# Kernel optimization log

Measured on AMD Instinct MI355X. Metric: run time of the kernel, lower is better.

## Reference

```python
import jax, jax.numpy as jnp
import numpy as np

EMB, HEADS, T_BLK = 1024, 16, 2048
B, T = 2, 2048
HD = EMB // HEADS


def setup_inputs() -> dict:
    key = jax.random.key(0)
    ks = jax.random.split(key, 9)
    s = 1.0 / np.sqrt(EMB)
    return {
        "x": jax.random.normal(ks[0], (B, T, EMB), jnp.float32),
        "Wq": jax.random.normal(ks[1], (EMB, EMB), jnp.float32) * s,
        "bq": jax.random.normal(ks[2], (EMB,), jnp.float32) * s,
        "Wk": jax.random.normal(ks[3], (EMB, EMB), jnp.float32) * s,
        "bk": jax.random.normal(ks[4], (EMB,), jnp.float32) * s,
        "Wv": jax.random.normal(ks[5], (EMB, EMB), jnp.float32) * s,
        "bv": jax.random.normal(ks[6], (EMB,), jnp.float32) * s,
        "Wo": jax.random.normal(ks[7], (EMB, EMB), jnp.float32) * s,
        "bo": jax.random.normal(ks[8], (EMB,), jnp.float32) * s,
    }


def reference(x, Wq, bq, Wk, bk, Wv, bv, Wo, bo):
    # eval mode: dropout is identity
    Bn, Tn, C = x.shape
    def proj(W, b):
        y = x @ W.T + b                      # [B,T,C]
        return y.reshape(Bn, Tn, HEADS, HD).transpose(0, 2, 1, 3)  # [B,H,T,hd]
    q, k, v = proj(Wq, bq), proj(Wk, bk), proj(Wv, bv)
    scores = jnp.einsum('bhqd,bhkd->bhqk', q, k) * (HD ** -0.5)  # [B,H,T,T]
    causal = jnp.tril(jnp.ones((Tn, Tn), dtype=bool))
    scores = jnp.where(causal, scores, -jnp.inf)
    w = jax.nn.softmax(scores, axis=-1)
    out = jnp.einsum('bhqk,bhkd->bhqd', w, v)                    # [B,H,T,hd]
    out = out.transpose(0, 2, 1, 3).reshape(Bn, Tn, C)
    return out @ Wo.T + bo
```

## Files before the change

kernel.cpp:

```cpp
#include <hip/hip_runtime.h>
#include <stdint.h>

#define EMB   1024
#define HEADS 16
#define HD    64
#define BB    2
#define TT    2048
#define MTOT  (BB*TT)
#define LDA   72

#define ELX (4194304u)
#define ELW (1048576u)

#define CSCALE (0.125f * 1.44269504088896f)

typedef __attribute__((ext_vector_type(8))) short short8;
typedef __attribute__((ext_vector_type(4))) float f32x4;
typedef __attribute__((ext_vector_type(4))) unsigned short us4;

__device__ __forceinline__ float bf2f(ushort u) {
  union { uint32_t u; float f; } x; x.u = ((uint32_t)u) << 16; return x.f;
}
__device__ __forceinline__ ushort f2bf(float f) {
  union { float f; uint32_t u; } x; x.f = f;
  uint32_t u = x.u;
  u += 0x7fffu + ((u >> 16) & 1u);
  return (ushort)(u >> 16);
}
__device__ __forceinline__ ushort f2bf_trunc(float f) {
  union { float f; uint32_t u; } x; x.f = f;
  return (ushort)(x.u >> 16);
}
__device__ __forceinline__ uint32_t pack2(uint32_t lo, uint32_t hi) {
  return (lo >> 16) | (hi & 0xFFFF0000u);
}
__device__ __forceinline__ short8 pack8(f32x4 a, f32x4 b) {
  union { f32x4 v; uint32_t u[4]; } A, B;
  A.v = a; B.v = b;
  union { uint32_t d[4]; short8 s; } R;
  R.d[0] = pack2(A.u[0], A.u[1]);
  R.d[1] = pack2(A.u[2], A.u[3]);
  R.d[2] = pack2(B.u[0], B.u[1]);
  R.d[3] = pack2(B.u[2], B.u[3]);
  return R.s;
}

__device__ __forceinline__ short8 cvt8_rne(const float* f) {
  f32x4 a = *(const f32x4*)f;
  f32x4 b = *(const f32x4*)(f + 4);
  short8 r;
  r[0] = (short)f2bf(a[0]); r[1] = (short)f2bf(a[1]);
  r[2] = (short)f2bf(a[2]); r[3] = (short)f2bf(a[3]);
  r[4] = (short)f2bf(b[0]); r[5] = (short)f2bf(b[1]);
  r[6] = (short)f2bf(b[2]); r[7] = (short)f2bf(b[3]);
  return r;
}

__global__ void detect_dtype(const uint32_t* __restrict__ x, int* __restrict__ flag) {
  if (threadIdx.x == 0) {
    int cnt = 0;
    for (int i = 0; i < 256; ++i) {
      uint32_t lo = x[i] & 0xFFFFu;
      uint32_t e = (lo >> 7) & 0xFFu;
      if (e >= 0x70u && e <= 0x8Fu) ++cnt;
    }
    *flag = (cnt > 128) ? 1 : 0;
  }
}

__global__ __launch_bounds__(256) void convert3(const void* __restrict__ w0,
                                                const void* __restrict__ w1,
                                                const void* __restrict__ w2,
                                                ushort* __restrict__ dst,
                                                const int* __restrict__ flag) {
  const size_t i = ((size_t)blockIdx.x * 256 + threadIdx.x) * 8;
  const int wi = (int)(i >> 20);
  const size_t off = i & (ELW - 1);
  const void* src = (wi == 0) ? w0 : (wi == 1) ? w1 : w2;
  if (*flag) *(short8*)(dst + i) = *(const short8*)((const ushort*)src + off);
  else       *(short8*)(dst + i) = cvt8_rne((const float*)src + off);
}

template<bool BF> struct PF {
  short8 b0, b1;
  f32x4 f0, f1, f2, f3;
  __device__ __forceinline__ void load(const void* base, size_t i0, size_t i1) {
    if constexpr (BF) {
      b0 = *(const short8*)((const ushort*)base + i0);
      b1 = *(const short8*)((const ushort*)base + i1);
    } else {
      const float* p0 = (const float*)base + i0;
      const float* p1 = (const float*)base + i1;
      f0 = *(const f32x4*)p0; f1 = *(const f32x4*)(p0 + 4);
      f2 = *(const f32x4*)p1; f3 = *(const f32x4*)(p1 + 4);
    }
  }
  __device__ __forceinline__ void store(ushort* l0, ushort* l1) {
    if constexpr (BF) { *(short8*)l0 = b0; *(short8*)l1 = b1; }
    else { *(short8*)l0 = pack8(f0, f1); *(short8*)l1 = pack8(f2, f3); }
  }
};

template<bool ABF, bool WBF>
__device__ __forceinline__ void gemm_pipe128(const void* __restrict__ Ap,
                                             const void* __restrict__ Bp,
                                             int m0, int n0,
                                             ushort* As, ushort* Ws,
                                             f32x4 acc[4][4]) {
  const int tid  = threadIdx.x;
  const int w    = tid >> 6;
  const int lane = tid & 63;
  const int quad = lane >> 4;
  const int l16  = lane & 15;
  const int wrow = w >> 1, wcol = w & 1;
  const int srow = tid >> 2;
  const int scol = (tid & 3) * 8;

  const size_t a0 = (size_t)(m0 + srow) * EMB + scol;
  const size_t a1 = (size_t)(m0 + srow + 64) * EMB + scol;
  const size_t b0 = (size_t)(n0 + srow) * EMB + scol;
  const size_t b1 = (size_t)(n0 + srow + 64) * EMB + scol;

  PF<ABF> pa; PF<WBF> pb;
  pa.load(Ap, a0, a1);
  pb.load(Bp, b0, b1);

  for (int k0 = 0; k0 < EMB; k0 += 32) {
    __syncthreads();
    pa.store(&As[srow * 32 + scol], &As[(srow + 64) * 32 + scol]);
    pb.store(&Ws[srow * 32 + scol], &Ws[(srow + 64) * 32 + scol]);
    if (k0 + 32 < EMB) {
      pa.load(Ap, a0 + k0 + 32, a1 + k0 + 32);
      pb.load(Bp, b0 + k0 + 32, b1 + k0 + 32);
    }
    __syncthreads();

    short8 af[4], bfr[4];
#pragma unroll
    for (int i = 0; i < 4; ++i)
      af[i]  = *(const short8*)&As[(wrow * 64 + i * 16 + l16) * 32 + quad * 8];
#pragma unroll
    for (int i = 0; i < 4; ++i)
      bfr[i] = *(const short8*)&Ws[(wcol * 64 + i * 16 + l16) * 32 + quad * 8];
#pragma unroll
    for (int mi = 0; mi < 4; ++mi)
#pragma unroll
      for (int ni = 0; ni < 4; ++ni)
        acc[mi][ni] = __builtin_amdgcn_mfma_f32_16x16x32_bf16(af[mi], bfr[ni], acc[mi][ni], 0, 0, 0);
  }
}

__device__ __forceinline__ void qkv_epilogue(f32x4 acc[4][4], int mt, int n0, int mat,
                                             const void* bias, int isbf,
                                             ushort* qo, ushort* ko, ushort* vo) {
  const int tid  = threadIdx.x;
  const int w    = tid >> 6;
  const int lane = tid & 63;
  const int quad = lane >> 4;
  const int l16  = lane & 15;
  const int wrow = w >> 1, wcol = w & 1;
  ushort* dst = (mat == 0) ? qo : ko;
  const float sc = (mat == 0) ? CSCALE : 1.0f;

#pragma unroll
  for (int ni = 0; ni < 4; ++ni) {
    const int n = n0 + wcol * 64 + ni * 16 + l16;
    const float bv_ = isbf ? bf2f(((const ushort*)bias)[n]) : ((const float*)bias)[n];
    const int hh = n >> 6, d = n & 63;
#pragma unroll
    for (int mi = 0; mi < 4; ++mi) {
      const int mbase = mt * 128 + wrow * 64 + mi * 16 + quad * 4;
      const int b = mbase >> 11, t = mbase & (TT - 1);
      if (mat == 2) {
        us4 pk;
#pragma unroll
        for (int r = 0; r < 4; ++r) pk[r] = f2bf(acc[mi][ni][r] + bv_);
        *(us4*)&vo[((size_t)((b * HEADS + hh) * HD + d)) * TT + t] = pk;
      } else {
#pragma unroll
        for (int r = 0; r < 4; ++r)
          dst[((size_t)((b * HEADS + hh) * TT + t + r)) * HD + d] = f2bf((acc[mi][ni][r] + bv_) * sc);
      }
    }
  }
}

__global__ __launch_bounds__(256) void qkv_pipe(const void* __restrict__ x,
                                                const ushort* __restrict__ w3,
                                                const void* __restrict__ bq,
                                                const void* __restrict__ bk,
                                                const void* __restrict__ bv,
                                                ushort* __restrict__ qo,
                                                ushort* __restrict__ ko,
                                                ushort* __restrict__ vo,
                                                const int* __restrict__ flag) {
  __shared__ __align__(16) ushort As[128 * 32];
  __shared__ __align__(16) ushort Ws[128 * 32];
  const int nt = blockIdx.x % 24;
  const int mt = blockIdx.x / 24;
  const int mat = nt >> 3;
  const int n0  = (nt & 7) * 128;
  const ushort* W  = w3 + (size_t)mat * ELW;
  const void* bias = (mat == 0) ? bq : (mat == 1) ? bk : bv;

  f32x4 acc[4][4];
#pragma unroll
  for (int i = 0; i < 4; ++i)
#pragma unroll
    for (int j = 0; j < 4; ++j) acc[i][j] = (f32x4){0.f, 0.f, 0.f, 0.f};

  const int isbf = *flag;
  if (isbf) gemm_pipe128<true,  true>(x, W, mt * 128, n0, As, Ws, acc);
  else      gemm_pipe128<false, true>(x, W, mt * 128, n0, As, Ws, acc);
  qkv_epilogue(acc, mt, n0, mat, bias, isbf, qo, ko, vo);
}

__global__ __launch_bounds__(256) void attn3(const ushort* __restrict__ qw,
                                             const ushort* __restrict__ kw,
                                             const ushort* __restrict__ vtw,
                                             ushort* __restrict__ out) {
  __shared__ __align__(16) ushort Ks[64 * LDA];
  __shared__ __align__(16) ushort Vts[64 * LDA];
  __shared__ __align__(16) ushort Ps[4][16 * LDA];

  const int bid = blockIdx.x;
  const int j  = bid >> 8;
  const int r8 = bid & 255;
  const int qh = r8 & 31;
  const int bh = j * 8 + (r8 >> 5);
  int qt;
  if      (j == 0) qt = qh;
  else if (j == 1) qt = 31 - qh;
  else if (j == 2) qt = (qh + 16) & 31;
  else             qt = 31 - ((qh + 16) & 31);
  const int h = bh & (HEADS - 1);
  const int b = bh >> 4;

  const int tid  = threadIdx.x;
  const int w    = tid >> 6;
  const int lane = tid & 63;
  const int quad = lane >> 4;
  const int l16  = lane & 15;

  const size_t hoff = ((size_t)(b * HEADS + h)) * TT * HD;
  const ushort* Qg = qw + hoff;
  const ushort* Kg = kw + hoff;
  const ushort* Vg = vtw + hoff;
  const int q0 = qt * 64;

  short8 qf[2];
  {
    const ushort* qrow = Qg + (size_t)(q0 + w * 16 + l16) * HD;
    qf[0] = *(const short8*)(qrow + quad * 8);
    qf[1] = *(const short8*)(qrow + 32 + quad * 8);
  }

  const int row = tid >> 2;
  const int c0  = (tid & 3) * 16;
  const ushort* Kbase = Kg + (size_t)row * HD + c0;
  const ushort* Vbase = Vg + (size_t)row * TT + c0;

  short8 pk0 = *(const short8*)(Kbase);
  short8 pk1 = *(const short8*)(Kbase + 8);
  short8 pv0 = *(const short8*)(Vbase);
  short8 pv1 = *(const short8*)(Vbase + 8);

  float ls[4] = {0.f, 0.f, 0.f, 0.f};
  f32x4 O[4];
#pragma unroll
  for (int ni = 0; ni < 4; ++ni) O[ni] = (f32x4){0.f, 0.f, 0.f, 0.f};

  for (int kt = 0; kt <= qt; ++kt) {
    const int k0 = kt * 64;
    __syncthreads();
    *(short8*)&Ks[row * LDA + c0]      = pk0;
    *(short8*)&Ks[row * LDA + c0 + 8]  = pk1;
    *(short8*)&Vts[row * LDA + c0]     = pv0;
    *(short8*)&Vts[row * LDA + c0 + 8] = pv1;
    if (kt < qt) {
      const size_t ko_ = (size_t)(k0 + 64) * HD;
      pk0 = *(const short8*)(Kbase + ko_);
      pk1 = *(const short8*)(Kbase + ko_ + 8);
      pv0 = *(const short8*)(Vbase + k0 + 64);
      pv1 = *(const short8*)(Vbase + k0 + 64 + 8);
    }
    __syncthreads();

    f32x4 s[4];
#pragma unroll
    for (int ni = 0; ni < 4; ++ni) s[ni] = (f32x4){0.f, 0.f, 0.f, 0.f};
#pragma unroll
    for (int ks = 0; ks < 2; ++ks) {
#pragma unroll
      for (int ni = 0; ni < 4; ++ni) {
        short8 kb = *(const short8*)&Ks[(ni * 16 + l16) * LDA + ks * 32 + quad * 8];
        s[ni] = __builtin_amdgcn_mfma_f32_16x16x32_bf16(qf[ks], kb, s[ni], 0, 0, 0);
      }
    }

    if (kt == qt) {
#pragma unroll
      for (int ni = 0; ni < 4; ++ni) {
        const int kk = k0 + ni * 16 + l16;
#pragma unroll
        for (int r = 0; r < 4; ++r) {
          const int qq = q0 + w * 16 + quad * 4 + r;
          if (kk > qq) s[ni][r] = -__builtin_inff();
        }
      }
    }

#pragma unroll
    for (int ni = 0; ni < 4; ++ni)
#pragma unroll
      for (int r = 0; r < 4; ++r) {
        const float p = exp2f(s[ni][r]);
        s[ni][r] = p;
        ls[r] += p;
      }

#pragma unroll
    for (int ni = 0; ni < 4; ++ni)
#pragma unroll
      for (int r = 0; r < 4; ++r)
        Ps[w][(quad * 4 + r) * LDA + ni * 16 + l16] = f2bf_trunc(s[ni][r]);

#pragma unroll
    for (int ks = 0; ks < 2; ++ks) {
      short8 a = *(const short8*)&Ps[w][l16 * LDA + ks * 32 + quad * 8];
#pragma unroll
      for (int ni = 0; ni < 4; ++ni) {
        short8 vb = *(const short8*)&Vts[(ni * 16 + l16) * LDA + ks * 32 + quad * 8];
        O[ni] = __builtin_amdgcn_mfma_f32_16x16x32_bf16(a, vb, O[ni], 0, 0, 0);
      }
    }
  }

#pragma unroll
  for (int r = 0; r < 4; ++r) {
#pragma unroll
    for (int off = 1; off < 16; off <<= 1) ls[r] += __shfl_xor(ls[r], off);
    const float inv = 1.0f / ls[r];
    const int t = q0 + w * 16 + quad * 4 + r;
#pragma unroll
    for (int ni = 0; ni < 4; ++ni) {
      out[((size_t)(b * TT + t)) * EMB + h * HD + ni * 16 + l16] = f2bf(O[ni][r] * inv);
    }
  }
}

template<bool WBF>
__device__ __forceinline__ void proj_core(const ushort* __restrict__ A,
                                          const void* __restrict__ Wo,
                                          int m0, int n0,
                                          ushort* As, ushort* Ws,
                                          f32x4 acc[4][2]) {
  const int tid  = threadIdx.x;
  const int w    = tid >> 6;
  const int lane = tid & 63;
  const int quad = lane >> 4;
  const int l16  = lane & 15;
  const int srow = tid >> 2;
  const int scol = (tid & 3) * 8;

  const size_t ai = (size_t)(m0 + srow) * EMB + scol;
  const size_t b0 = (size_t)(n0 + srow) * EMB + scol;
  const size_t b1 = (size_t)(n0 + srow + 64) * EMB + scol;

  short8 pa;
  PF<WBF> pb;
  pa = *(const short8*)(A + ai);
  pb.load(Wo, b0, b1);

  for (int k0 = 0; k0 < EMB; k0 += 32) {
    __syncthreads();
    *(short8*)&As[srow * 32 + scol] = pa;
    pb.store(&Ws[srow * 32 + scol], &Ws[(srow + 64) * 32 + scol]);
    if (k0 + 32 < EMB) {
      pa = *(const short8*)(A + ai + k0 + 32);
      pb.load(Wo, b0 + k0 + 32, b1 + k0 + 32);
    }
    __syncthreads();

    short8 af[4], bfr[2];
#pragma unroll
    for (int i = 0; i < 4; ++i)
      af[i]  = *(const short8*)&As[(i * 16 + l16) * 32 + quad * 8];
#pragma unroll
    for (int i = 0; i < 2; ++i)
      bfr[i] = *(const short8*)&Ws[(w * 32 + i * 16 + l16) * 32 + quad * 8];
#pragma unroll
    for (int mi = 0; mi < 4; ++mi)
#pragma unroll
      for (int ni = 0; ni < 2; ++ni)
        acc[mi][ni] = __builtin_amdgcn_mfma_f32_16x16x32_bf16(af[mi], bfr[ni], acc[mi][ni], 0, 0, 0);
  }
}

__global__ __launch_bounds__(256) void proj_pipe(const ushort* __restrict__ A,
                                                 const void* __restrict__ Wo,
                                                 const void* __restrict__ bo,
                                                 void* __restrict__ out,
                                                 const int* __restrict__ flag) {
  __shared__ __align__(16) ushort As[64 * 32];
  __shared__ __align__(16) ushort Ws[128 * 32];
  const int nt = blockIdx.x & 7;
  const int mt = blockIdx.x >> 3;
  const int n0 = nt * 128;
  const int m0 = mt * 64;

  f32x4 acc[4][2];
#pragma unroll
  for (int i = 0; i < 4; ++i)
#pragma unroll
    for (int jj = 0; jj < 2; ++jj) acc[i][jj] = (f32x4){0.f, 0.f, 0.f, 0.f};

  const int isbf = *flag;
  if (isbf) proj_core<true >(A, Wo, m0, n0, As, Ws, acc);
  else      proj_core<false>(A, Wo, m0, n0, As, Ws, acc);

  const int tid  = threadIdx.x;
  const int w    = tid >> 6;
  const int lane = tid & 63;
  const int quad = lane >> 4;
  const int l16  = lane & 15;

#pragma unroll
  for (int ni = 0; ni < 2; ++ni) {
    const int n = n0 + w * 32 + ni * 16 + l16;
    const float bv_ = isbf ? bf2f(((const ushort*)bo)[n]) : ((const float*)bo)[n];
#pragma unroll
    for (int mi = 0; mi < 4; ++mi) {
#pragma unroll
      for (int r = 0; r < 4; ++r) {
        const int m = m0 + mi * 16 + quad * 4 + r;
        const float v = acc[mi][ni][r] + bv_;
        if (isbf) ((ushort*)out)[(size_t)m * EMB + n] = f2bf(v);
        else      ((float*) out)[(size_t)m * EMB + n] = v;
      }
    }
  }
}

extern "C" void kernel_launch(void* const* d_in, const int* in_sizes, int n_in,
                              void* d_out, int out_size, void* d_ws, size_t ws_size,
                              hipStream_t stream) {
  const void* x  = d_in[0];
  const void* Wq = d_in[1];
  const void* bq = d_in[2];
  const void* Wk = d_in[3];
  const void* bk = d_in[4];
  const void* Wv = d_in[5];
  const void* bv = d_in[6];
  const void* Wo = d_in[7];
  const void* bo = d_in[8];

  int* flag = (int*)d_ws;
  ushort* base = (ushort*)((char*)d_ws + 256);

  ushort* q_ws  = base;
  ushort* k_ws  = q_ws + ELX;
  ushort* vt_ws = k_ws + ELX;
  ushort* w3    = vt_ws + ELX;
  ushort* o_ws  = vt_ws + ELX;

  detect_dtype<<<dim3(1), dim3(64), 0, stream>>>((const uint32_t*)x, flag);
  convert3<<<dim3(1536), dim3(256), 0, stream>>>(Wq, Wk, Wv, w3, flag);
  qkv_pipe<<<dim3(768), dim3(256), 0, stream>>>(x, w3, bq, bk, bv,
                                                q_ws, k_ws, vt_ws, flag);
  attn3<<<dim3(1024), dim3(256), 0, stream>>>(q_ws, k_ws, vt_ws, o_ws);
  proj_pipe<<<dim3(512), dim3(256), 0, stream>>>(o_ws, Wo, bo, d_out, flag);
}
```

Before: 227.8 us.

## Retile QKV GEMM to 64x128 tiles with BK=64 and XCD-aware block mapping

Result: no change. 228.2 us (+0.1%).

```diff
diff --git a/kernel.cpp b/kernel.cpp
--- a/kernel.cpp
+++ b/kernel.cpp
@@ -8,6 +8,7 @@
 #define TT    2048
 #define MTOT  (BB*TT)
 #define LDA   72
+#define LDP   72
 
 #define ELX (4194304u)
 #define ELW (1048576u)
@@ -44,7 +45,6 @@
   R.d[3] = pack2(B.u[2], B.u[3]);
   return R.s;
 }
-
 __device__ __forceinline__ short8 cvt8_rne(const float* f) {
   f32x4 a = *(const f32x4*)f;
   f32x4 b = *(const f32x4*)(f + 4);
@@ -81,95 +81,100 @@
   else       *(short8*)(dst + i) = cvt8_rne((const float*)src + off);
 }
 
-template<bool BF> struct PF {
-  short8 b0, b1;
-  f32x4 f0, f1, f2, f3;
-  __device__ __forceinline__ void load(const void* base, size_t i0, size_t i1) {
-    if constexpr (BF) {
-      b0 = *(const short8*)((const ushort*)base + i0);
-      b1 = *(const short8*)((const ushort*)base + i1);
-    } else {
-      const float* p0 = (const float*)base + i0;
-      const float* p1 = (const float*)base + i1;
-      f0 = *(const f32x4*)p0; f1 = *(const f32x4*)(p0 + 4);
-      f2 = *(const f32x4*)p1; f3 = *(const f32x4*)(p1 + 4);
-    }
-  }
-  __device__ __forceinline__ void store(ushort* l0, ushort* l1) {
-    if constexpr (BF) { *(short8*)l0 = b0; *(short8*)l1 = b1; }
-    else { *(short8*)l0 = pack8(f0, f1); *(short8*)l1 = pack8(f2, f3); }
-  }
-};
-
-template<bool ABF, bool WBF>
-__device__ __forceinline__ void gemm_pipe128(const void* __restrict__ Ap,
-                                             const void* __restrict__ Bp,
-                                             int m0, int n0,
-                                             ushort* As, ushort* Ws,
-                                             f32x4 acc[4][4]) {
+template<bool ABF>
+__device__ __forceinline__ void gemm_qkv64(const void* __restrict__ Ap,
+                                           const ushort* __restrict__ Wp,
+                                           int m0, int n0,
+                                           ushort* As, ushort* Ws,
+                                           f32x4 acc[4][2]) {
   const int tid  = threadIdx.x;
   const int w    = tid >> 6;
   const int lane = tid & 63;
   const int quad = lane >> 4;
   const int l16  = lane & 15;
-  const int wrow = w >> 1, wcol = w & 1;
-  const int srow = tid >> 2;
-  const int scol = (tid & 3) * 8;
-
-  const size_t a0 = (size_t)(m0 + srow) * EMB + scol;
-  const size_t a1 = (size_t)(m0 + srow + 64) * EMB + scol;
-  const size_t b0 = (size_t)(n0 + srow) * EMB + scol;
-  const size_t b1 = (size_t)(n0 + srow + 64) * EMB + scol;
-
-  PF<ABF> pa; PF<WBF> pb;
-  pa.load(Ap, a0, a1);
-  pb.load(Bp, b0, b1);
-
-  for (int k0 = 0; k0 < EMB; k0 += 32) {
+  const int arow = tid >> 2;
+  const int acol = (tid & 3) * 16;
+  const int brow = tid >> 1;
+  const int bcol = (tid & 1) * 32;
+
+  const size_t aoff = (size_t)(m0 + arow) * EMB + acol;
+  const size_t boff = (size_t)(n0 + brow) * EMB + bcol;
+
+  short8 ab[2];
+  f32x4  af[4];
+  short8 wb[4];
+  if constexpr (ABF) {
+    ab[0] = *(const short8*)((const ushort*)Ap + aoff);
+    ab[1] = *(const short8*)((const ushort*)Ap + aoff + 8);
+  } else {
+#pragma unroll
+    for (int i = 0; i < 4; ++i) af[i] = *(const f32x4*)((const float*)Ap + aoff + 4 * i);
+  }
+#pragma unroll
+  for (int i = 0; i < 4; ++i) wb[i] = *(const short8*)(Wp + boff + 8 * i);
+
+  for (int k0 = 0; k0 < EMB; k0 += 64) {
     __syncthreads();
-    pa.store(&As[srow * 32 + scol], &As[(srow + 64) * 32 + scol]);
-    pb.store(&Ws[srow * 32 + scol], &Ws[(srow + 64) * 32 + scol]);
-    if (k0 + 32 < EMB) {
-      pa.load(Ap, a0 + k0 + 32, a1 + k0 + 32);
-      pb.load(Bp, b0 + k0 + 32, b1 + k0 + 32);
+    if constexpr (ABF) {
+      *(short8*)&As[arow * LDP + acol]     = ab[0];
+      *(short8*)&As[arow * LDP + acol + 8] = ab[1];
+    } else {
+      *(short8*)&As[arow * LDP + acol]     = pack8(af[0], af[1]);
+      *(short8*)&As[arow * LDP + acol + 8] = pack8(af[2], af[3]);
+    }
+#pragma unroll
+    for (int i = 0; i < 4; ++i) *(short8*)&Ws[brow * LDP + bcol + 8 * i] = wb[i];
+    if (k0 + 64 < EMB) {
+      if constexpr (ABF) {
+        ab[0] = *(const short8*)((const ushort*)Ap + aoff + k0 + 64);
+        ab[1] = *(const short8*)((const ushort*)Ap + aoff + k0 + 64 + 8);
+      } else {
+#pragma unroll
+        for (int i = 0; i < 4; ++i)
+          af[i] = *(const f32x4*)((const float*)Ap + aoff + k0 + 64 + 4 * i);
+      }
+#pragma unroll
+      for (int i = 0; i < 4; ++i) wb[i] = *(const short8*)(Wp + boff + k0 + 64 + 8 * i);
     }
     __syncthreads();
 
-    short8 af[4], bfr[4];
-#pragma unroll
-    for (int i = 0; i < 4; ++i)
-      af[i]  = *(const short8*)&As[(wrow * 64 + i * 16 + l16) * 32 + quad * 8];
-#pragma unroll
-    for (int i = 0; i < 4; ++i)
-      bfr[i] = *(const short8*)&Ws[(wcol * 64 + i * 16 + l16) * 32 + quad * 8];
-#pragma unroll
-    for (int mi = 0; mi < 4; ++mi)
-#pragma unroll
-      for (int ni = 0; ni < 4; ++ni)
-        acc[mi][ni] = __builtin_amdgcn_mfma_f32_16x16x32_bf16(af[mi], bfr[ni], acc[mi][ni], 0, 0, 0);
-  }
-}
-
-__device__ __forceinline__ void qkv_epilogue(f32x4 acc[4][4], int mt, int n0, int mat,
-                                             const void* bias, int isbf,
-                                             ushort* qo, ushort* ko, ushort* vo) {
+#pragma unroll
+    for (int ks = 0; ks < 2; ++ks) {
+      short8 a_[4], b_[2];
+#pragma unroll
+      for (int i = 0; i < 4; ++i)
+        a_[i] = *(const short8*)&As[(i * 16 + l16) * LDP + ks * 32 + quad * 8];
+#pragma unroll
+      for (int i = 0; i < 2; ++i)
+        b_[i] = *(const short8*)&Ws[(w * 32 + i * 16 + l16) * LDP + ks * 32 + quad * 8];
+#pragma unroll
+      for (int mi = 0; mi < 4; ++mi)
+#pragma unroll
+        for (int ni = 0; ni < 2; ++ni)
+          acc[mi][ni] = __builtin_amdgcn_mfma_f32_16x16x32_bf16(a_[mi], b_[ni], acc[mi][ni], 0, 0, 0);
+    }
+  }
+}
+
+__device__ __forceinline__ void qkv_epi64(f32x4 acc[4][2], int mt, int n0, int mat,
+                                          const void* bias, int isbf,
+                                          ushort* qo, ushort* ko, ushort* vo) {
   const int tid  = threadIdx.x;
   const int w    = tid >> 6;
   const int lane = tid & 63;
   const int quad = lane >> 4;
   const int l16  = lane & 15;
-  const int wrow = w >> 1, wcol = w & 1;
   ushort* dst = (mat == 0) ? qo : ko;
   const float sc = (mat == 0) ? CSCALE : 1.0f;
 
 #pragma unroll
-  for (int ni = 0; ni < 4; ++ni) {
-    const int n = n0 + wcol * 64 + ni * 16 + l16;
+  for (int ni = 0; ni < 2; ++ni) {
+    const int n = n0 + w * 32 + ni * 16 + l16;
     const float bv_ = isbf ? bf2f(((const ushort*)bias)[n]) : ((const float*)bias)[n];
     const int hh = n >> 6, d = n & 63;
 #pragma unroll
     for (int mi = 0; mi < 4; ++mi) {
-      const int mbase = mt * 128 + wrow * 64 + mi * 16 + quad * 4;
+      const int mbase = mt * 64 + mi * 16 + quad * 4;
       const int b = mbase >> 11, t = mbase & (TT - 1);
       if (mat == 2) {
         us4 pk;
@@ -194,25 +199,27 @@
                                                 ushort* __restrict__ ko,
                                                 ushort* __restrict__ vo,
                                                 const int* __restrict__ flag) {
-  __shared__ __align__(16) ushort As[128 * 32];
-  __shared__ __align__(16) ushort Ws[128 * 32];
-  const int nt = blockIdx.x % 24;
-  const int mt = blockIdx.x / 24;
+  __shared__ __align__(16) ushort As[64 * LDP];
+  __shared__ __align__(16) ushort Ws[128 * LDP];
+  const int xcd = blockIdx.x & 7;
+  const int i   = blockIdx.x >> 3;
+  const int nt  = xcd * 3 + (i % 3);
+  const int mt  = i / 3;
   const int mat = nt >> 3;
   const int n0  = (nt & 7) * 128;
   const ushort* W  = w3 + (size_t)mat * ELW;
   const void* bias = (mat == 0) ? bq : (mat == 1) ? bk : bv;
 
-  f32x4 acc[4][4];
-#pragma unroll
-  for (int i = 0; i < 4; ++i)
-#pragma unroll
-    for (int j = 0; j < 4; ++j) acc[i][j] = (f32x4){0.f, 0.f, 0.f, 0.f};
+  f32x4 acc[4][2];
+#pragma unroll
+  for (int a = 0; a < 4; ++a)
+#pragma unroll
+    for (int b = 0; b < 2; ++b) acc[a][b] = (f32x4){0.f, 0.f, 0.f, 0.f};
 
   const int isbf = *flag;
-  if (isbf) gemm_pipe128<true,  true>(x, W, mt * 128, n0, As, Ws, acc);
-  else      gemm_pipe128<false, true>(x, W, mt * 128, n0, As, Ws, acc);
-  qkv_epilogue(acc, mt, n0, mat, bias, isbf, qo, ko, vo);
+  if (isbf) gemm_qkv64<true >(x, W, mt * 64, n0, As, Ws, acc);
+  else      gemm_qkv64<false>(x, W, mt * 64, n0, As, Ws, acc);
+  qkv_epi64(acc, mt, n0, mat, bias, isbf, qo, ko, vo);
 }
 
 __global__ __launch_bounds__(256) void attn3(const ushort* __restrict__ qw,
@@ -349,6 +356,26 @@
   }
 }
 
+template<bool BF> struct PF {
+  short8 b0, b1;
+  f32x4 f0, f1, f2, f3;
+  __device__ __forceinline__ void load(const void* base, size_t i0, size_t i1) {
+    if constexpr (BF) {
+      b0 = *(const short8*)((const ushort*)base + i0);
+      b1 = *(const short8*)((const ushort*)base + i1);
+    } else {
+      const float* p0 = (const float*)base + i0;
+      const float* p1 = (const float*)base + i1;
+      f0 = *(const f32x4*)p0; f1 = *(const f32x4*)(p0 + 4);
+      f2 = *(const f32x4*)p1; f3 = *(const f32x4*)(p1 + 4);
+    }
+  }
+  __device__ __forceinline__ void store(ushort* l0, ushort* l1) {
+    if constexpr (BF) { *(short8*)l0 = b0; *(short8*)l1 = b1; }
+    else { *(short8*)l0 = pack8(f0, f1); *(short8*)l1 = pack8(f2, f3); }
+  }
+};
+
 template<bool WBF>
 __device__ __forceinline__ void proj_core(const ushort* __restrict__ A,
                                           const void* __restrict__ Wo,
@@ -466,8 +493,8 @@
 
   detect_dtype<<<dim3(1), dim3(64), 0, stream>>>((const uint32_t*)x, flag);
   convert3<<<dim3(1536), dim3(256), 0, stream>>>(Wq, Wk, Wv, w3, flag);
-  qkv_pipe<<<dim3(768), dim3(256), 0, stream>>>(x, w3, bq, bk, bv,
-                                                q_ws, k_ws, vt_ws, flag);
+  qkv_pipe<<<dim3(1536), dim3(256), 0, stream>>>(x, w3, bq, bk, bv,
+                                                 q_ws, k_ws, vt_ws, flag);
   attn3<<<dim3(1024), dim3(256), 0, stream>>>(q_ws, k_ws, vt_ws, o_ws);
   proj_pipe<<<dim3(512), dim3(256), 0, stream>>>(o_ws, Wo, bo, d_out, flag);
 }
```
